# Performance work log

Hardware: AMD Instinct MI355X
Metric: run time of the kernel (lower is better)

The kernel has to match this reference:

```python
import jax, jax.numpy as jnp
import numpy as np

EPS = 1e-6

def gram_schmidt_orthonormalize(U, eps=EPS):
    # U: [B, K, D] -> orthonormalized along K, vectorized over batch
    B, K, D = U.shape
    vs = []
    for i in range(K):
        v = U[:, i]  # [B, D]
        for vj in vs:
            coeff = jnp.sum(v * vj, axis=1, keepdims=True) / (jnp.sum(vj * vj, axis=1, keepdims=True) + eps)
            v = v - coeff * vj
        norm = jnp.maximum(jnp.linalg.norm(v, axis=1, keepdims=True), eps)
        vs.append(v / norm)
    return jnp.stack(vs, axis=1)  # [B, K, D]

def setup_inputs() -> dict:
    key = jax.random.key(0)
    ks = jax.random.split(key, 14)
    B, IN, H1, H2, OUT, E, G = 4096, 1024, 2048, 2048, 512, 8, 256
    s = 0.02
    return {
        "x":   jax.random.normal(ks[0], (B, IN), jnp.float32),
        "W1":  jax.random.normal(ks[1], (E, IN, H1), jnp.float32) * s,
        "b1":  jnp.zeros((E, H1), jnp.float32),
        "W2":  jax.random.normal(ks[2], (E, H1, H2), jnp.float32) * s,
        "b2":  jnp.zeros((E, H2), jnp.float32),
        "W3":  jax.random.normal(ks[3], (E, H2, OUT), jnp.float32) * s,
        "b3":  jnp.zeros((E, OUT), jnp.float32),
        "Wg1": jax.random.normal(ks[4], (IN, G), jnp.float32) * s,
        "bg1": jnp.zeros((G,), jnp.float32),
        "Wg2": jax.random.normal(ks[5], (G, E), jnp.float32) * s,
        "bg2": jnp.zeros((E,), jnp.float32),
        "Wo":  jax.random.normal(ks[6], (OUT, 1), jnp.float32) * s,
        "bo":  jnp.zeros((1,), jnp.float32),
    }

def reference(x, W1, b1, W2, b2, W3, b3, Wg1, bg1, Wg2, bg2, Wo, bo):
    # Expert MLPs, batched over expert axis e: [B,E,h]
    h = jax.nn.relu(jnp.einsum('bi,eih->beh', x, W1) + b1)
    h = jax.nn.relu(jnp.einsum('beh,ehk->bek', h, W2) + b2)
    expert_outputs = jnp.einsum('bek,ekd->bed', h, W3) + b3  # [B, E, D]
    # Gating network: MLP + softmax over experts
    g = jax.nn.relu(x @ Wg1 + bg1)
    gate_weights = jax.nn.softmax(g @ Wg2 + bg2, axis=-1)  # [B, E]
    # Per-sample Gram-Schmidt across experts, weighted combine
    ortho = gram_schmidt_orthonormalize(expert_outputs)  # [B, E, D]
    combined = jnp.einsum('bed,be->bd', ortho, gate_weights)  # [B, D]
    final = combined @ Wo + bo  # [B, 1]
    return (final, 0.0)
```

## Files before the change

kernel.cpp:

```cpp
#include <hip/hip_runtime.h>
#include <hip/hip_bf16.h>

#define DEVINL __device__ __forceinline__

constexpr int Bsz = 4096, INF = 1024, H1 = 2048, H2 = 2048, OUTD = 512, NE = 8, G = 256;

typedef __attribute__((ext_vector_type(8))) short bf16x8;
typedef __attribute__((ext_vector_type(4))) float f32x4;
typedef __attribute__((ext_vector_type(16))) float f32x16;
typedef unsigned short u16;

DEVINL u16 f2bf(float f) {
  unsigned int u = __float_as_uint(f);
  u = (u + 0x7FFFu + ((u >> 16) & 1u)) >> 16;
  return (u16)u;
}
DEVINL float bf2f(u16 h) { return __uint_as_float((unsigned int)h << 16); }

DEVINL void gload16(const void* g, void* l) {
  __builtin_amdgcn_global_load_lds(
      (const __attribute__((address_space(1))) void*)g,
      (__attribute__((address_space(3))) void*)l, 16, 0, 0);
}

DEVINL float waveAllSum(float v) {
#pragma unroll
  for (int m = 32; m > 0; m >>= 1) v += __shfl_xor(v, m, 64);
  return v;
}

DEVINL f32x16 mfma3(bf16x8 bh, bf16x8 bl, bf16x8 ah, bf16x8 al, f32x16 c) {
  c = __builtin_amdgcn_mfma_f32_32x32x16_bf16(bh, ah, c, 0, 0, 0);
  c = __builtin_amdgcn_mfma_f32_32x32x16_bf16(bl, ah, c, 0, 0, 0);
  c = __builtin_amdgcn_mfma_f32_32x32x16_bf16(bh, al, c, 0, 0, 0);
  return c;
}

__global__ __launch_bounds__(256) void pack_wt(const float* __restrict__ W,
                                               u16* __restrict__ Th,
                                               u16* __restrict__ Tl,
                                               int K, int N) {
  __shared__ float t[32][33];
  const int e = blockIdx.z;
  W += (size_t)e * K * N;
  Th += (size_t)e * N * K;
  Tl += (size_t)e * N * K;
  const int n0 = blockIdx.x * 32, k0 = blockIdx.y * 32;
  const int r = threadIdx.x >> 3, c = (threadIdx.x & 7) * 4;
  float4 v = *(const float4*)&W[(size_t)(k0 + r) * N + n0 + c];
  t[r][c + 0] = v.x; t[r][c + 1] = v.y; t[r][c + 2] = v.z; t[r][c + 3] = v.w;
  __syncthreads();
  float o0 = t[c + 0][r], o1 = t[c + 1][r], o2 = t[c + 2][r], o3 = t[c + 3][r];
  short4 h, l;
  h.x = f2bf(o0); l.x = f2bf(o0 - bf2f(h.x));
  h.y = f2bf(o1); l.y = f2bf(o1 - bf2f(h.y));
  h.z = f2bf(o2); l.z = f2bf(o2 - bf2f(h.z));
  h.w = f2bf(o3); l.w = f2bf(o3 - bf2f(h.w));
  *(short4*)&Th[(size_t)(n0 + r) * K + k0 + c] = h;
  *(short4*)&Tl[(size_t)(n0 + r) * K + k0 + c] = l;
}

__global__ __launch_bounds__(512, 2) void gemm_2bar(
    const u16* __restrict__ Ahi, const u16* __restrict__ Alo,
    const u16* __restrict__ Bhi, const u16* __restrict__ Blo,
    const float* __restrict__ bias,
    u16* __restrict__ Chi, u16* __restrict__ Clo,
    int M, int N, int K, size_t strideAe) {
  const int e = blockIdx.x;
  Ahi += (size_t)e * strideAe;
  Alo += (size_t)e * strideAe;
  Bhi += (size_t)e * (size_t)N * K;
  Blo += (size_t)e * (size_t)N * K;
  bias += (size_t)e * N;
  Chi += (size_t)e * (size_t)M * N;
  Clo += (size_t)e * (size_t)M * N;

  const int bm = blockIdx.y * 256, bn = blockIdx.z * 256;
  __shared__ __align__(16) char ldsb[131072];
  const int lane = threadIdx.x & 63, wid = threadIdx.x >> 6;
  const int wm = wid >> 2, wn = wid & 3;
  const int l15 = lane & 15, l4 = lane >> 4;
  const int bhalf = wn >> 1, jn = wn & 1;

  f32x4 acc[8][4];
#pragma unroll
  for (int i = 0; i < 8; ++i)
#pragma unroll
    for (int j = 0; j < 4; ++j) acc[i][j] = (f32x4){0.f, 0.f, 0.f, 0.f};

  const int nt = K / 32;

  auto stageA = [&](const u16* src, int T, int ldsOp) {
    const int s = T & 1;
#pragma unroll
    for (int q = 0; q < 2; ++q) {
      const int g = wid * 2 + q;
      gload16(src + (size_t)(bm + g * 16 + l15) * K + T * 32 + l4 * 8,
              ldsb + ldsOp + s * 16384 + g * 1024);
    }
  };
  auto stageB = [&](int T, int h) {
    const int s = T & 1;
#pragma unroll
    for (int q = 0; q < 2; ++q) {
      const int g = wid * 2 + q;
      const u16* src = (g < 8) ? Bhi : Blo;
      const int f = g & 7;
      gload16(src + (size_t)(bn + h * 128 + f * 16 + l15) * K + T * 32 + l4 * 8,
              ldsb + ((g < 8) ? 65536 : 98304) + s * 16384 + h * 8192 + f * 1024);
    }
  };

  bf16x8 ah[4], al[4], bh[4], bl[4];
  auto readA = [&](int s, int ih) {
#pragma unroll
    for (int i = 0; i < 4; ++i) {
      const int off = s * 16384 + wm * 8192 + (ih * 4 + i) * 1024 + lane * 16;
      ah[i] = *(const bf16x8*)(ldsb + off);
      al[i] = *(const bf16x8*)(ldsb + 32768 + off);
    }
  };
  auto readBall = [&](int s) {
#pragma unroll
    for (int j = 0; j < 4; ++j) {
      const int off = s * 16384 + bhalf * 8192 + (jn * 4 + j) * 1024 + lane * 16;
      bh[j] = *(const bf16x8*)(ldsb + 65536 + off);
      bl[j] = *(const bf16x8*)(ldsb + 98304 + off);
    }
  };

#define QUAD48(IH)                                                             \
  _Pragma("unroll") for (int i = 0; i < 4; ++i) {                              \
    _Pragma("unroll") for (int j = 0; j < 4; ++j) {                            \
      f32x4 a = acc[(IH)*4 + i][j];                                            \
      a = __builtin_amdgcn_mfma_f32_16x16x32_bf16(bh[j], ah[i], a, 0, 0, 0);   \
      a = __builtin_amdgcn_mfma_f32_16x16x32_bf16(bl[j], ah[i], a, 0, 0, 0);   \
      a = __builtin_amdgcn_mfma_f32_16x16x32_bf16(bh[j], al[i], a, 0, 0, 0);   \
      acc[(IH)*4 + i][j] = a;                                                  \
    }                                                                          \
  }

  stageB(0, 0); stageB(0, 1);
  stageA(Ahi, 0, 0); stageA(Alo, 0, 32768);
  stageB(1, 0); stageB(1, 1);
  asm volatile("s_waitcnt vmcnt(4)" ::: "memory");
  __builtin_amdgcn_sched_barrier(0);
  __builtin_amdgcn_s_barrier();
  __builtin_amdgcn_sched_barrier(0);

  for (int t = 0; t < nt - 2; ++t) {
    const int s = t & 1;
    readA(s, 0);
    readBall(s);
    __builtin_amdgcn_sched_barrier(0);
    stageA(Ahi, t + 1, 0); stageA(Alo, t + 1, 32768);
    QUAD48(0);
    __builtin_amdgcn_sched_barrier(0);
    __builtin_amdgcn_s_barrier();
    __builtin_amdgcn_sched_barrier(0);
    readA(s, 1);
    __builtin_amdgcn_sched_barrier(0);
    stageB(t + 2, 0); stageB(t + 2, 1);
    QUAD48(1);
    asm volatile("s_waitcnt vmcnt(4)" ::: "memory");
    __builtin_amdgcn_sched_barrier(0);
    __builtin_amdgcn_s_barrier();
    __builtin_amdgcn_sched_barrier(0);
  }
  {
    const int s = (nt - 2) & 1;
    readA(s, 0);
    readBall(s);
    __builtin_amdgcn_sched_barrier(0);
    stageA(Ahi, nt - 1, 0); stageA(Alo, nt - 1, 32768);
    QUAD48(0);
    __builtin_amdgcn_sched_barrier(0);
    __builtin_amdgcn_s_barrier();
    __builtin_amdgcn_sched_barrier(0);
    readA(s, 1);
    QUAD48(1);
    asm volatile("s_waitcnt vmcnt(0)" ::: "memory");
    __builtin_amdgcn_sched_barrier(0);
    __builtin_amdgcn_s_barrier();
    __builtin_amdgcn_sched_barrier(0);
  }
  {
    const int s = (nt - 1) & 1;
    readA(s, 0);
    readBall(s);
    QUAD48(0);
    readA(s, 1);
    QUAD48(1);
  }
#undef QUAD48

#pragma unroll
  for (int i = 0; i < 8; ++i) {
    const int grow = bm + wm * 128 + i * 16 + l15;
#pragma unroll
    for (int j = 0; j < 4; ++j) {
      const int gcol = bn + wn * 64 + j * 16 + l4 * 4;
      const float4 bb = *(const float4*)&bias[gcol];
      float v0 = fmaxf(acc[i][j][0] + bb.x, 0.f);
      float v1 = fmaxf(acc[i][j][1] + bb.y, 0.f);
      float v2 = fmaxf(acc[i][j][2] + bb.z, 0.f);
      float v3 = fmaxf(acc[i][j][3] + bb.w, 0.f);
      short4 h, l;
      h.x = f2bf(v0); l.x = f2bf(v0 - bf2f(h.x));
      h.y = f2bf(v1); l.y = f2bf(v1 - bf2f(h.y));
      h.z = f2bf(v2); l.z = f2bf(v2 - bf2f(h.z));
      h.w = f2bf(v3); l.w = f2bf(v3 - bf2f(h.w));
      *(short4*)&Chi[(size_t)grow * N + gcol] = h;
      *(short4*)&Clo[(size_t)grow * N + gcol] = l;
    }
  }
}

__global__ __launch_bounds__(512, 2) void gemm32_128(
    const u16* __restrict__ Ahi, const u16* __restrict__ Alo,
    const u16* __restrict__ Bhi, const u16* __restrict__ Blo,
    const float* __restrict__ bias, float* __restrict__ Cf,
    int M, int N, int K, size_t strideAe) {
  const int e = blockIdx.x;
  Ahi += (size_t)e * strideAe;
  Alo += (size_t)e * strideAe;
  Bhi += (size_t)e * (size_t)N * K;
  Blo += (size_t)e * (size_t)N * K;
  bias += (size_t)e * N;
  Cf += (size_t)e * (size_t)M * N;

  const int bm = blockIdx.y * 128, bn = blockIdx.z * 256;
  __shared__ __align__(16) char ldsb[131072];
  const int lane = threadIdx.x & 63, wid = threadIdx.x >> 6;
  const int wm = wid >> 2, wn = wid & 3;
  const int l31 = lane & 31, lk = lane >> 5;

  f32x16 acc[2][2];
#pragma unroll
  for (int i = 0; i < 2; ++i)
#pragma unroll
    for (int j = 0; j < 2; ++j)
#pragma unroll
      for (int q = 0; q < 16; ++q) acc[i][j][q] = 0.f;

  const int nt = K / 32;

  auto stageA2 = [&](int T) {
    const int s = T & 1;
#pragma unroll
    for (int q = 0; q < 2; ++q) {
      const int g = wid * 2 + q;
      const u16* src = (g < 8) ? Ahi : Alo;
      const int f = g & 7;
      gload16(src + (size_t)(bm + (f >> 1) * 32 + l31) * K + T * 32 + (f & 1) * 16 + lk * 8,
              ldsb + ((g < 8) ? 0 : 16384) + s * 8192 + f * 1024);
    }
  };
  auto stageB2 = [&](int T, int slot) {
#pragma unroll
    for (int q = 0; q < 4; ++q) {
      const int g = wid * 4 + q;
      const u16* src = (g < 16) ? Bhi : Blo;
      const int f = g & 15;
      gload16(src + (size_t)(bn + (f >> 1) * 32 + l31) * K + T * 32 + (f & 1) * 16 + lk * 8,
              ldsb + ((g < 16) ? 32768 : 81920) + slot * 16384 + f * 1024);
    }
  };

  bf16x8 ah[2][2], al[2][2], b0h[2], b0l[2], b1h[2], b1l[2];
  auto readA2 = [&](int s) {
#pragma unroll
    for (int i = 0; i < 2; ++i)
#pragma unroll
      for (int ks = 0; ks < 2; ++ks) {
        const int off = s * 8192 + ((wm * 2 + i) * 2 + ks) * 1024 + lane * 16;
        ah[i][ks] = *(const bf16x8*)(ldsb + off);
        al[i][ks] = *(const bf16x8*)(ldsb + 16384 + off);
      }
  };
  auto readB2 = [&](int bs, int jh, bf16x8* bh, bf16x8* bl) {
#pragma unroll
    for (int ks = 0; ks < 2; ++ks) {
      const int off = bs * 16384 + ((wn * 2 + jh) * 2 + ks) * 1024 + lane * 16;
      bh[ks] = *(const bf16x8*)(ldsb + 32768 + off);
      bl[ks] = *(const bf16x8*)(ldsb + 81920 + off);
    }
  };

#define QUAD2(JH, BH, BL)                                                   \
  _Pragma("unroll") for (int i = 0; i < 2; ++i) {                           \
    _Pragma("unroll") for (int ks = 0; ks < 2; ++ks) {                      \
      acc[i][JH] = mfma3(BH[ks], BL[ks], ah[i][ks], al[i][ks], acc[i][JH]); \
    }                                                                       \
  }

  stageA2(0);
  stageB2(0, 0);
  stageB2(1, 1);
  asm volatile("s_waitcnt vmcnt(4)" ::: "memory");
  __builtin_amdgcn_sched_barrier(0);
  __builtin_amdgcn_s_barrier();
  __builtin_amdgcn_sched_barrier(0);

  int bs = 0;
  for (int t = 0; t < nt - 2; ++t) {
    const int sa = t & 1;
    int bs2 = bs - 1; if (bs2 < 0) bs2 = 2;
    readA2(sa);
    readB2(bs, 0, b0h, b0l);
    readB2(bs, 1, b1h, b1l);
    __builtin_amdgcn_sched_barrier(0);
    stageA2(t + 1);
    stageB2(t + 2, bs2);
    QUAD2(0, b0h, b0l);
    QUAD2(1, b1h, b1l);
    asm volatile("s_waitcnt vmcnt(4)" ::: "memory");
    __builtin_amdgcn_sched_barrier(0);
    __builtin_amdgcn_s_barrier();
    __builtin_amdgcn_sched_barrier(0);
    bs = (bs == 2) ? 0 : bs + 1;
  }
  {
    const int sa = (nt - 2) & 1;
    readA2(sa);
    readB2(bs, 0, b0h, b0l);
    readB2(bs, 1, b1h, b1l);
    __builtin_amdgcn_sched_barrier(0);
    stageA2(nt - 1);
    QUAD2(0, b0h, b0l);
    QUAD2(1, b1h, b1l);
    asm volatile("s_waitcnt vmcnt(0)" ::: "memory");
    __builtin_amdgcn_sched_barrier(0);
    __builtin_amdgcn_s_barrier();
    __builtin_amdgcn_sched_barrier(0);
    bs = (bs == 2) ? 0 : bs + 1;
  }
  {
    const int sa = (nt - 1) & 1;
    readA2(sa);
    readB2(bs, 0, b0h, b0l);
    readB2(bs, 1, b1h, b1l);
    QUAD2(0, b0h, b0l);
    QUAD2(1, b1h, b1l);
  }
#undef QUAD2

#pragma unroll
  for (int rt = 0; rt < 2; ++rt) {
    const int grow = bm + wm * 64 + rt * 32 + l31;
#pragma unroll
    for (int ct = 0; ct < 2; ++ct) {
      const int gcol0 = bn + wn * 64 + ct * 32;
      const f32x16 a = acc[rt][ct];
#pragma unroll
      for (int q = 0; q < 4; ++q) {
        const int c0 = gcol0 + q * 8 + lk * 4;
        const float4 bb = *(const float4*)&bias[c0];
        *(float4*)&Cf[(size_t)grow * N + c0] =
            make_float4(a[q * 4 + 0] + bb.x, a[q * 4 + 1] + bb.y,
                        a[q * 4 + 2] + bb.z, a[q * 4 + 3] + bb.w);
      }
    }
  }
}

__global__ __launch_bounds__(256) void gate1_kernel(
    const float* __restrict__ x, const float* __restrict__ Wg1,
    const float* __restrict__ bg1, float* __restrict__ g,
    u16* __restrict__ xhi, u16* __restrict__ xlo) {
  __shared__ float xs[8 * 1024];
  const int b0 = blockIdx.x * 8;
  const size_t base = (size_t)b0 * INF;
  const float* xp = x + base;
  for (int idx = threadIdx.x * 4; idx < 8 * 1024; idx += 1024) {
    float4 v = *(const float4*)&xp[idx];
    *(float4*)&xs[idx] = v;
    short4 h, l;
    h.x = f2bf(v.x); l.x = f2bf(v.x - bf2f(h.x));
    h.y = f2bf(v.y); l.y = f2bf(v.y - bf2f(h.y));
    h.z = f2bf(v.z); l.z = f2bf(v.z - bf2f(h.z));
    h.w = f2bf(v.w); l.w = f2bf(v.w - bf2f(h.w));
    *(short4*)&xhi[base + idx] = h;
    *(short4*)&xlo[base + idx] = l;
  }
  __syncthreads();
  const int t = threadIdx.x;
  float acc[8] = {0, 0, 0, 0, 0, 0, 0, 0};
  for (int i = 0; i < INF; ++i) {
    float w = Wg1[(size_t)i * G + t];
#pragma unroll
    for (int r = 0; r < 8; ++r) acc[r] = fmaf(xs[r * 1024 + i], w, acc[r]);
  }
  const float bb = bg1[t];
#pragma unroll
  for (int r = 0; r < 8; ++r)
    g[(size_t)(b0 + r) * G + t] = fmaxf(acc[r] + bb, 0.0f);
}

__global__ __launch_bounds__(64) void gate2_kernel(
    const float* __restrict__ g, const float* __restrict__ Wg2,
    const float* __restrict__ bg2, float* __restrict__ gw) {
  const int b = blockIdx.x, lane = threadIdx.x;
  float4 gv = *(const float4*)(g + (size_t)b * G + lane * 4);
  float p[8];
#pragma unroll
  for (int e = 0; e < 8; ++e) {
    int j = lane * 4;
    float s = gv.x * Wg2[(j + 0) * 8 + e] + gv.y * Wg2[(j + 1) * 8 + e] +
              gv.z * Wg2[(j + 2) * 8 + e] + gv.w * Wg2[(j + 3) * 8 + e];
    p[e] = waveAllSum(s);
  }
  if (lane == 0) {
    float l[8];
    float mx = -1e30f;
#pragma unroll
    for (int e = 0; e < 8; ++e) {
      l[e] = p[e] + bg2[e];
      mx = fmaxf(mx, l[e]);
    }
    float sum = 0.0f;
#pragma unroll
    for (int e = 0; e < 8; ++e) {
      l[e] = expf(l[e] - mx);
      sum += l[e];
    }
    float inv = 1.0f / sum;
#pragma unroll
    for (int e = 0; e < 8; ++e) gw[(size_t)b * 8 + e] = l[e] * inv;
  }
}

__global__ __launch_bounds__(256) void gs_kernel(
    const float* __restrict__ eo, const float* __restrict__ gw,
    const float* __restrict__ Wo, const float* __restrict__ bo,
    float* __restrict__ out, int CB) {
  const int lane = threadIdx.x & 63;
  const int b = blockIdx.x * 4 + (threadIdx.x >> 6);
  const size_t ES = (size_t)CB * OUTD;
  const float* base = eo + (size_t)b * OUTD + lane * 8;
  float vs[8][8];
  float denom[8];
#pragma unroll
  for (int i = 0; i < 8; ++i) {
    float cur[8];
    float4 u0 = *(const float4*)(base + (size_t)i * ES);
    float4 u1 = *(const float4*)(base + (size_t)i * ES + 4);
    cur[0] = u0.x; cur[1] = u0.y; cur[2] = u0.z; cur[3] = u0.w;
    cur[4] = u1.x; cur[5] = u1.y; cur[6] = u1.z; cur[7] = u1.w;
#pragma unroll
    for (int j = 0; j < i; ++j) {
      float dp = 0.0f;
#pragma unroll
      for (int d = 0; d < 8; ++d) dp = fmaf(cur[d], vs[j][d], dp);
      dp = waveAllSum(dp);
      float coeff = dp / (denom[j] + 1e-6f);
#pragma unroll
      for (int d = 0; d < 8; ++d) cur[d] = fmaf(-coeff, vs[j][d], cur[d]);
    }
    float nn = 0.0f;
#pragma unroll
    for (int d = 0; d < 8; ++d) nn = fmaf(cur[d], cur[d], nn);
    nn = waveAllSum(nn);
    float inv = 1.0f / fmaxf(sqrtf(nn), 1e-6f);
#pragma unroll
    for (int d = 0; d < 8; ++d) vs[i][d] = cur[d] * inv;
    float dd = 0.0f;
#pragma unroll
    for (int d = 0; d < 8; ++d) dd = fmaf(vs[i][d], vs[i][d], dd);
    denom[i] = waveAllSum(dd);
  }
  float gwv[8];
#pragma unroll
  for (int e = 0; e < 8; ++e) gwv[e] = gw[(size_t)b * 8 + e];
  float part = 0.0f;
#pragma unroll
  for (int d = 0; d < 8; ++d) {
    float c = 0.0f;
#pragma unroll
    for (int e = 0; e < 8; ++e) c = fmaf(vs[e][d], gwv[e], c);
    part = fmaf(c, Wo[lane * 8 + d], part);
  }
  part = waveAllSum(part);
  if (lane == 0) out[b] = part + bo[0];
}

extern "C" void kernel_launch(void* const* d_in, const int* in_sizes, int n_in,
                              void* d_out, int out_size, void* d_ws, size_t ws_size,
                              hipStream_t stream) {
  const float* x   = (const float*)d_in[0];
  const float* W1  = (const float*)d_in[1];
  const float* b1  = (const float*)d_in[2];
  const float* W2  = (const float*)d_in[3];
  const float* b2  = (const float*)d_in[4];
  const float* W3  = (const float*)d_in[5];
  const float* b3  = (const float*)d_in[6];
  const float* Wg1 = (const float*)d_in[7];
  const float* bg1 = (const float*)d_in[8];
  const float* Wg2 = (const float*)d_in[9];
  const float* bg2 = (const float*)d_in[10];
  const float* Wo  = (const float*)d_in[11];
  const float* bo  = (const float*)d_in[12];
  float* out = (float*)d_out;

  char* p = (char*)d_ws;
  float* gw = (float*)p;          p += (size_t)(128u << 10);
  float* g  = (float*)p;          p += (size_t)(4u << 20);
  u16* xhi = (u16*)p;             p += (size_t)Bsz * INF * 2;
  u16* xlo = (u16*)p;             p += (size_t)Bsz * INF * 2;
  u16* w1h = (u16*)p;             p += (size_t)NE * H1 * INF * 2;
  u16* w1l = (u16*)p;             p += (size_t)NE * H1 * INF * 2;
  u16* w2h = (u16*)p;             p += (size_t)NE * H2 * H1 * 2;
  u16* w2l = (u16*)p;             p += (size_t)NE * H2 * H1 * 2;
  u16* w3h = (u16*)p;             p += (size_t)NE * OUTD * H2 * 2;
  u16* w3l = (u16*)p;             p += (size_t)NE * OUTD * H2 * 2;
  const size_t fixedBytes = (size_t)(p - (char*)d_ws);

  int CB = 4096;
  while (CB > 256 && fixedBytes + (size_t)CB * (size_t)(128u << 10) > ws_size) CB >>= 1;
  u16* h1h = (u16*)p;
  u16* h1l = h1h + (size_t)NE * CB * H1;
  u16* h2h = h1l + (size_t)NE * CB * H1;
  u16* h2l = h2h + (size_t)NE * CB * H2;
  float* eo = (float*)h1h;

  hipMemsetAsync(d_out, 0, (size_t)out_size * sizeof(float), stream);

  gate1_kernel<<<Bsz / 8, 256, 0, stream>>>(x, Wg1, bg1, g, xhi, xlo);
  gate2_kernel<<<Bsz, 64, 0, stream>>>(g, Wg2, bg2, gw);

  pack_wt<<<dim3(H1 / 32, INF / 32, NE), 256, 0, stream>>>(W1, w1h, w1l, INF, H1);
  pack_wt<<<dim3(H2 / 32, H1 / 32, NE), 256, 0, stream>>>(W2, w2h, w2l, H1, H2);
  pack_wt<<<dim3(OUTD / 32, H2 / 32, NE), 256, 0, stream>>>(W3, w3h, w3l, H2, OUTD);

  for (int c0 = 0; c0 < Bsz; c0 += CB) {
    gemm_2bar<<<dim3(NE, CB / 256, H1 / 256), 512, 0, stream>>>(
        xhi + (size_t)c0 * INF, xlo + (size_t)c0 * INF, w1h, w1l, b1,
        h1h, h1l, CB, H1, INF, (size_t)0);
    gemm_2bar<<<dim3(NE, CB / 256, H2 / 256), 512, 0, stream>>>(
        h1h, h1l, w2h, w2l, b2, h2h, h2l, CB, H2, H1, (size_t)CB * H1);
    gemm32_128<<<dim3(NE, CB / 128, OUTD / 256), 512, 0, stream>>>(
        h2h, h2l, w3h, w3l, b3, eo, CB, OUTD, H2, (size_t)CB * H2);
    gs_kernel<<<CB / 4, 256, 0, stream>>>(eo, gw + (size_t)c0 * NE, Wo, bo,
                                          out + c0, CB);
  }
}
```

Measured before the change: 1.564 ms.

## Triple-buffer A tiles in LDS to prefetch two K-steps ahead

The expert GEMM's A operand (hi and lo parts) moves from a double-buffered to a triple-buffered LDS ring, growing shared memory from 128 KB to 160 KB per block. A tiles are now issued two iterations ahead, and the vmcnt wait thresholds are raised to match the extra loads in flight. This aims to hide more global-load latency behind the MFMA work and drops one barrier in the tail. The cost is that each block now uses the full 160 KB of LDS, and the hand-tuned wait counts and slot rotation must stay exactly consistent.

```diff
diff --git a/kernel.cpp b/kernel.cpp
--- a/kernel.cpp
+++ b/kernel.cpp
@@ -76,7 +76,7 @@
   Clo += (size_t)e * (size_t)M * N;
 
   const int bm = blockIdx.y * 256, bn = blockIdx.z * 256;
-  __shared__ __align__(16) char ldsb[131072];
+  __shared__ __align__(16) char ldsb[163840];
   const int lane = threadIdx.x & 63, wid = threadIdx.x >> 6;
   const int wm = wid >> 2, wn = wid & 3;
   const int l15 = lane & 15, l4 = lane >> 4;
@@ -90,13 +90,12 @@
 
   const int nt = K / 32;
 
-  auto stageA = [&](const u16* src, int T, int ldsOp) {
-    const int s = T & 1;
+  auto stageA = [&](const u16* src, int T, int slot, int ldsOp) {
 #pragma unroll
     for (int q = 0; q < 2; ++q) {
       const int g = wid * 2 + q;
       gload16(src + (size_t)(bm + g * 16 + l15) * K + T * 32 + l4 * 8,
-              ldsb + ldsOp + s * 16384 + g * 1024);
+              ldsb + ldsOp + slot * 16384 + g * 1024);
     }
   };
   auto stageB = [&](int T, int h) {
@@ -107,25 +106,25 @@
       const u16* src = (g < 8) ? Bhi : Blo;
       const int f = g & 7;
       gload16(src + (size_t)(bn + h * 128 + f * 16 + l15) * K + T * 32 + l4 * 8,
-              ldsb + ((g < 8) ? 65536 : 98304) + s * 16384 + h * 8192 + f * 1024);
+              ldsb + ((g < 8) ? 98304 : 131072) + s * 16384 + h * 8192 + f * 1024);
     }
   };
 
   bf16x8 ah[4], al[4], bh[4], bl[4];
-  auto readA = [&](int s, int ih) {
+  auto readA = [&](int slot, int ih) {
 #pragma unroll
     for (int i = 0; i < 4; ++i) {
-      const int off = s * 16384 + wm * 8192 + (ih * 4 + i) * 1024 + lane * 16;
+      const int off = slot * 16384 + wm * 8192 + (ih * 4 + i) * 1024 + lane * 16;
       ah[i] = *(const bf16x8*)(ldsb + off);
-      al[i] = *(const bf16x8*)(ldsb + 32768 + off);
-    }
-  };
-  auto readBall = [&](int s) {
+      al[i] = *(const bf16x8*)(ldsb + 49152 + off);
+    }
+  };
+  auto readBall = [&](int sB) {
 #pragma unroll
     for (int j = 0; j < 4; ++j) {
-      const int off = s * 16384 + bhalf * 8192 + (jn * 4 + j) * 1024 + lane * 16;
-      bh[j] = *(const bf16x8*)(ldsb + 65536 + off);
-      bl[j] = *(const bf16x8*)(ldsb + 98304 + off);
+      const int off = sB * 16384 + bhalf * 8192 + (jn * 4 + j) * 1024 + lane * 16;
+      bh[j] = *(const bf16x8*)(ldsb + 98304 + off);
+      bl[j] = *(const bf16x8*)(ldsb + 131072 + off);
     }
   };
 
@@ -141,55 +140,55 @@
   }
 
   stageB(0, 0); stageB(0, 1);
-  stageA(Ahi, 0, 0); stageA(Alo, 0, 32768);
+  stageA(Ahi, 0, 0, 0); stageA(Alo, 0, 0, 49152);
   stageB(1, 0); stageB(1, 1);
-  asm volatile("s_waitcnt vmcnt(4)" ::: "memory");
+  stageA(Ahi, 1, 1, 0); stageA(Alo, 1, 1, 49152);
+  asm volatile("s_waitcnt vmcnt(8)" ::: "memory");
   __builtin_amdgcn_sched_barrier(0);
   __builtin_amdgcn_s_barrier();
   __builtin_amdgcn_sched_barrier(0);
 
+  int aS = 0, aS2 = 2;
   for (int t = 0; t < nt - 2; ++t) {
-    const int s = t & 1;
-    readA(s, 0);
-    readBall(s);
-    __builtin_amdgcn_sched_barrier(0);
-    stageA(Ahi, t + 1, 0); stageA(Alo, t + 1, 32768);
+    const int sB = t & 1;
+    readA(aS, 0);
+    readBall(sB);
+    __builtin_amdgcn_sched_barrier(0);
+    stageA(Ahi, t + 2, aS2, 0); stageA(Alo, t + 2, aS2, 49152);
     QUAD48(0);
     __builtin_amdgcn_sched_barrier(0);
     __builtin_amdgcn_s_barrier();
     __builtin_amdgcn_sched_barrier(0);
-    readA(s, 1);
+    readA(aS, 1);
     __builtin_amdgcn_sched_barrier(0);
     stageB(t + 2, 0); stageB(t + 2, 1);
     QUAD48(1);
-    asm volatile("s_waitcnt vmcnt(4)" ::: "memory");
+    asm volatile("s_waitcnt vmcnt(8)" ::: "memory");
     __builtin_amdgcn_sched_barrier(0);
     __builtin_amdgcn_s_barrier();
     __builtin_amdgcn_sched_barrier(0);
+    aS = (aS == 2) ? 0 : aS + 1;
+    aS2 = (aS2 == 2) ? 0 : aS2 + 1;
   }
   {
-    const int s = (nt - 2) & 1;
-    readA(s, 0);
-    readBall(s);
-    __builtin_amdgcn_sched_barrier(0);
-    stageA(Ahi, nt - 1, 0); stageA(Alo, nt - 1, 32768);
+    const int sB = (nt - 2) & 1;
+    readA(aS, 0);
+    readBall(sB);
     QUAD48(0);
-    __builtin_amdgcn_sched_barrier(0);
-    __builtin_amdgcn_s_barrier();
-    __builtin_amdgcn_sched_barrier(0);
-    readA(s, 1);
+    readA(aS, 1);
     QUAD48(1);
     asm volatile("s_waitcnt vmcnt(0)" ::: "memory");
     __builtin_amdgcn_sched_barrier(0);
     __builtin_amdgcn_s_barrier();
     __builtin_amdgcn_sched_barrier(0);
+    aS = (aS == 2) ? 0 : aS + 1;
   }
   {
-    const int s = (nt - 1) & 1;
-    readA(s, 0);
-    readBall(s);
+    const int sB = (nt - 1) & 1;
+    readA(aS, 0);
+    readBall(sB);
     QUAD48(0);
-    readA(s, 1);
+    readA(aS, 1);
     QUAD48(1);
   }
 #undef QUAD48
```

Result: no change. 1.555 ms (-0.5%).
